# Performance work log

Hardware: AMD Instinct MI355X
Metric: run time of the kernel (lower is better)

The kernel has to match this reference:

```python
import jax, jax.numpy as jnp
import numpy as np

DIM = 1024
HEADS = 16
HEAD_DIM = DIM // HEADS          # 64
ROT_DIM = max(16, HEAD_DIM // 2) # 32 (already even)
B, S = 1, 2048


def _linear_params(key, scale=0.02):
    w = jax.random.normal(key, (DIM, DIM), dtype=jnp.float32) * scale
    b = jnp.zeros((DIM,), dtype=jnp.float32)
    return w, b


def setup_inputs() -> dict:
    key = jax.random.key(0)
    ks = jax.random.split(key, 16)
    real = jax.random.normal(ks[0], (B, S, DIM), dtype=jnp.float32)
    imag = jax.random.normal(ks[1], (B, S, DIM), dtype=jnp.float32)
    Wq_r, bq_r = _linear_params(ks[2])
    Wk_r, bk_r = _linear_params(ks[3])
    Wv_r, bv_r = _linear_params(ks[4])
    Wq_i, bq_i = _linear_params(ks[5])
    Wk_i, bk_i = _linear_params(ks[6])
    Wv_i, bv_i = _linear_params(ks[7])
    Wo_r, bo_r = _linear_params(ks[8])
    Wo_i, bo_i = _linear_params(ks[9])
    phase_shifts = jax.random.normal(ks[10], (HEADS, HEAD_DIM), dtype=jnp.float32) * 0.02
    # entanglement init: 0.8*I + 0.1 on super/sub diagonal + 0.1 corners
    ent = np.eye(HEADS, dtype=np.float32) * 0.8
    ent += np.diag(np.ones(HEADS - 1, dtype=np.float32) * 0.1, k=1)
    ent += np.diag(np.ones(HEADS - 1, dtype=np.float32) * 0.1, k=-1)
    ent[0, -1] = 0.1
    ent[-1, 0] = 0.1
    entanglement_matrix = jnp.asarray(ent)
    exponent = np.arange(0, ROT_DIM, 2, dtype=np.float64) / ROT_DIM
    rotary_freqs = jnp.asarray((10000.0 ** (-exponent)).astype(np.float32))
    return {
        'real': real, 'imag': imag,
        'Wq_r': Wq_r, 'bq_r': bq_r, 'Wk_r': Wk_r, 'bk_r': bk_r,
        'Wv_r': Wv_r, 'bv_r': bv_r, 'Wq_i': Wq_i, 'bq_i': bq_i,
        'Wk_i': Wk_i, 'bk_i': bk_i, 'Wv_i': Wv_i, 'bv_i': bv_i,
        'Wo_r': Wo_r, 'bo_r': bo_r, 'Wo_i': Wo_i, 'bo_i': bo_i,
        'phase_shifts': phase_shifts,
        'entanglement_matrix': entanglement_matrix,
        'rotary_freqs': rotary_freqs,
        'interference_strength': jnp.float32(0.0),
        'attention_temperature': jnp.float32(0.0),
        'circle_epsilon': jnp.float32(-2.0),
    }


def _proj(x, W, b):
    # nn.Linear: x @ W^T + b, then split heads -> [B,H,S,Dh]
    y = x @ W.T + b
    return y.reshape(B, S, HEADS, HEAD_DIM).transpose(0, 2, 1, 3)


def _rope(x, cos, sin):
    # x: [B,H,S,Dh]; interleaved pairs rotated over first ROT_DIM dims
    xr, xp = x[..., :ROT_DIM], x[..., ROT_DIM:]
    x1, x2 = xr[..., 0::2], xr[..., 1::2]          # [B,H,S,ROT_DIM//2]
    o1 = x1 * cos - x2 * sin
    o2 = x1 * sin + x2 * cos
    out = jnp.stack([o1, o2], axis=-1).reshape(x.shape[:-1] + (ROT_DIM,))
    return jnp.concatenate([out, xp], axis=-1)


def reference(real, imag, Wq_r, bq_r, Wk_r, bk_r, Wv_r, bv_r,
              Wq_i, bq_i, Wk_i, bk_i, Wv_i, bv_i,
              Wo_r, bo_r, Wo_i, bo_i,
              phase_shifts, entanglement_matrix, rotary_freqs,
              interference_strength, attention_temperature, circle_epsilon):
    q_r = _proj(real, Wq_r, bq_r)
    k_r = _proj(real, Wk_r, bk_r)
    v_r = _proj(real, Wv_r, bv_r)
    q_i = _proj(imag, Wq_i, bq_i)
    k_i = _proj(imag, Wk_i, bk_i)
    v_i = _proj(imag, Wv_i, bv_i)

    # rotary embeddings
    pos = jnp.arange(S, dtype=jnp.float32)
    angles = jnp.outer(pos, rotary_freqs)              # [S, ROT_DIM//2]
    cos = jnp.cos(angles)[None, None]                  # [1,1,S,ROT_DIM//2]
    sin = jnp.sin(angles)[None, None]
    q_r = _rope(q_r, cos, sin); k_r = _rope(k_r, cos, sin)
    q_i = _rope(q_i, cos, sin); k_i = _rope(k_i, cos, sin)

    # entanglement mixing across heads
    q_r = jnp.einsum('bhsd,hx->bxsd', q_r, entanglement_matrix)
    q_i = jnp.einsum('bhsd,hx->bxsd', q_i, entanglement_matrix)
    k_r = jnp.einsum('bhsd,hx->bxsd', k_r, entanglement_matrix)
    k_i = jnp.einsum('bhsd,hx->bxsd', k_i, entanglement_matrix)

    # per-head learned phase shift
    pc = jnp.cos(phase_shifts)[None, :, None, :]       # [1,H,1,Dh]
    ps = jnp.sin(phase_shifts)[None, :, None, :]
    q_r, q_i = q_r * pc - q_i * ps, q_r * ps + q_i * pc
    k_r, k_i = k_r * pc - k_i * ps, k_r * ps + k_i * pc

    # complex attention scores (Karatsuba, as in HAKMEMComplexOperations)
    scale = 1.0 / np.sqrt(HEAD_DIM)
    k1 = jnp.einsum('bhsd,bhtd->bhst', q_r, k_r)
    k2 = jnp.einsum('bhsd,bhtd->bhst', q_i, k_i)
    k3 = jnp.einsum('bhsd,bhtd->bhst', q_r + q_i, k_r + k_i)
    attn_r = (k1 - k2) * scale
    attn_i = (k3 - k1 - k2) * scale

    eps = jax.nn.sigmoid(circle_epsilon) * 0.03
    ar = attn_r + eps * attn_i
    ai = attn_i - eps * attn_r
    attn_mag = jnp.sqrt(ar * ar + ai * ai + 1e-6)

    causal = jnp.triu(jnp.ones((S, S), dtype=bool), k=1)[None, None]
    attn_mag = jnp.where(causal, -jnp.inf, attn_mag)

    temp = jnp.clip(jnp.exp(attention_temperature), 0.1, None)
    strength = jax.nn.sigmoid(interference_strength)
    attn = jax.nn.softmax(attn_mag * strength / temp, axis=-1)
    attn = jnp.nan_to_num(attn)

    # complex_matmul(attn, 0, v_r, v_i) -> (attn@v_r, attn@v_i)
    out_r = jnp.einsum('bhst,bhtd->bhsd', attn, v_r)
    out_i = jnp.einsum('bhst,bhtd->bhsd', attn, v_i)
    out_r = out_r.transpose(0, 2, 1, 3).reshape(B, S, DIM)
    out_i = out_i.transpose(0, 2, 1, 3).reshape(B, S, DIM)
    out_r = out_r @ Wo_r.T + bo_r
    out_i = out_i @ Wo_i.T + bo_i
    return out_r, out_i
```

## Files before the change

### kernel.cpp

```cpp
#include <hip/hip_runtime.h>
#include <cstddef>
#include <cstdint>
#include <math.h>

#define S_LEN 2048
#define DIM 1024
#define NH 16
#define HD 64

typedef __attribute__((ext_vector_type(8))) short bf16x8;
typedef __attribute__((ext_vector_type(8))) unsigned short u16x8;
typedef __attribute__((ext_vector_type(4))) float f32x4;

__device__ inline unsigned short f2bf(float x) {
  union { float f; unsigned u; } v; v.f = x;
  unsigned r = v.u + 0x7FFFu + ((v.u >> 16) & 1u);
  return (unsigned short)(r >> 16);
}
__device__ inline float bf2f(unsigned short x) {
  union { unsigned u; float f; } v; v.u = ((unsigned)x) << 16; return v.f;
}

#define GLOAD_LDS16(g, l)                                              \
  __builtin_amdgcn_global_load_lds(                                    \
      (const __attribute__((address_space(1))) void*)(g),              \
      (__attribute__((address_space(3))) void*)(l), 16, 0, 0)

struct ConvBatch {
  const float* src[10];
  unsigned short* dst[10];
  int n[10];
};

__global__ __launch_bounds__(256) void conv_kernel(ConvBatch cb)
{
  const int y = blockIdx.y;
  const int i = (blockIdx.x * 256 + threadIdx.x) * 8;
  if (i >= cb.n[y]) return;
  const float* s = cb.src[y];
  float4 a = *(const float4*)(s + i);
  float4 b = *(const float4*)(s + i + 4);
  u16x8 o;
  o[0] = f2bf(a.x); o[1] = f2bf(a.y); o[2] = f2bf(a.z); o[3] = f2bf(a.w);
  o[4] = f2bf(b.x); o[5] = f2bf(b.y); o[6] = f2bf(b.z); o[7] = f2bf(b.w);
  *(u16x8*)(cb.dst[y] + i) = o;
}

struct BGemm {
  const unsigned short* A[6];
  const unsigned short* W[6];
  const float* bias[6];
  void* C[6];
  int mode[6];
};

__global__ __launch_bounds__(256) void gemm_mfma_kernel(BGemm gb)
{
  constexpr int K = DIM;
  const int z = blockIdx.z;
  const unsigned short* __restrict__ A = gb.A[z];
  const unsigned short* __restrict__ W = gb.W[z];
  const float* __restrict__ bias = gb.bias[z];
  const int mode = gb.mode[z];

  __shared__ __align__(16) unsigned short As[128 * 32];
  __shared__ __align__(16) unsigned short Ws[128 * 32];

  const int t    = threadIdx.x;
  const int lane = t & 63;
  const int w    = t >> 6;
  const int wm   = w >> 1, wn = w & 1;
  const int quad = lane >> 4, lcol = lane & 15;
  const int m0   = blockIdx.y * 128;
  const int n0   = blockIdx.x * 128;

  const int srow = t >> 2;
  const int sk8  = (t & 3) * 8;

  f32x4 acc[4][4];
#pragma unroll
  for (int i = 0; i < 4; i++)
#pragma unroll
    for (int j = 0; j < 4; j++)
#pragma unroll
      for (int r = 0; r < 4; r++) acc[i][j][r] = 0.f;

  for (int k0 = 0; k0 < K; k0 += 32) {
    __syncthreads();
#pragma unroll
    for (int p = 0; p < 2; p++) {
      const unsigned short* ga = A + (size_t)(m0 + p * 64 + srow) * K + k0 + sk8;
      GLOAD_LDS16(ga, As + (size_t)(p * 256 + w * 64) * 8);
      const unsigned short* gw = W + (size_t)(n0 + p * 64 + srow) * K + k0 + sk8;
      GLOAD_LDS16(gw, Ws + (size_t)(p * 256 + w * 64) * 8);
    }
    __syncthreads();

    bf16x8 af[4], bfr[4];
#pragma unroll
    for (int mi = 0; mi < 4; mi++)
      af[mi] = *(const bf16x8*)&As[(wm * 64 + mi * 16 + lcol) * 32 + quad * 8];
#pragma unroll
    for (int ni = 0; ni < 4; ni++)
      bfr[ni] = *(const bf16x8*)&Ws[(wn * 64 + ni * 16 + lcol) * 32 + quad * 8];
#pragma unroll
    for (int mi = 0; mi < 4; mi++)
#pragma unroll
      for (int ni = 0; ni < 4; ni++)
        acc[mi][ni] = __builtin_amdgcn_mfma_f32_16x16x32_bf16(af[mi], bfr[ni], acc[mi][ni], 0, 0, 0);
  }

#pragma unroll
  for (int mi = 0; mi < 4; mi++) {
#pragma unroll
    for (int ni = 0; ni < 4; ni++) {
#pragma unroll
      for (int r = 0; r < 4; r++) {
        const int grow = m0 + wm * 64 + mi * 16 + quad * 4 + r;
        const int gcol = n0 + wn * 64 + ni * 16 + lcol;
        const float v = acc[mi][ni][r] + bias[gcol];
        if (mode == 0) {
          ((float*)gb.C[z])[(size_t)grow * DIM + gcol] = v;
        } else if (mode == 1) {
          const int hh = gcol >> 6, d = gcol & 63;
          ((unsigned short*)gb.C[z])[((size_t)hh * S_LEN + grow) * HD + d] = f2bf(v);
        } else {
          const int hh = gcol >> 6, d = gcol & 63;
          ((unsigned short*)gb.C[z])[((size_t)hh * HD + d) * S_LEN + grow] = f2bf(v);
        }
      }
    }
  }
}

__global__ __launch_bounds__(256) void rope_kernel(
    unsigned short* q_r, unsigned short* k_r,
    unsigned short* q_i, unsigned short* k_i,
    const float* __restrict__ freqs)
{
  const int gid = blockIdx.x * 256 + threadIdx.x;
  const int j  = gid & 15;
  const int s  = (gid >> 4) & (S_LEN - 1);
  const int h  = (gid >> 15) & (NH - 1);
  const int tz = gid >> 19;
  unsigned short* buf = (tz == 0) ? q_r : (tz == 1) ? k_r : (tz == 2) ? q_i : k_i;

  const float ang = (float)s * freqs[j];
  float sn, cs;
  sincosf(ang, &sn, &cs);

  const size_t base = ((size_t)h * S_LEN + s) * HD + 2 * j;
  ushort2 xv = *(const ushort2*)(buf + base);
  const float x1 = bf2f(xv.x), x2 = bf2f(xv.y);
  ushort2 ov;
  ov.x = f2bf(x1 * cs - x2 * sn);
  ov.y = f2bf(x1 * sn + x2 * cs);
  *(ushort2*)(buf + base) = ov;
}

__global__ __launch_bounds__(256) void entangle_kernel(
    const unsigned short* __restrict__ qr_in, const unsigned short* __restrict__ qi_in,
    unsigned short* __restrict__ qr_out, unsigned short* __restrict__ qi_out,
    const unsigned short* __restrict__ kr_in, const unsigned short* __restrict__ ki_in,
    unsigned short* __restrict__ kr_out, unsigned short* __restrict__ ki_out,
    const float* __restrict__ E, const float* __restrict__ phase)
{
  const int z = blockIdx.z;
  const unsigned short* inR = z ? kr_in : qr_in;
  const unsigned short* inI = z ? ki_in : qi_in;
  unsigned short* outR = z ? kr_out : qr_out;
  unsigned short* outI = z ? ki_out : qi_out;

  __shared__ float Es[NH * NH];
  const int t = threadIdx.x;
  Es[t] = E[t];
  __syncthreads();

  const int idx = blockIdx.x * 256 + t;
  const int s = idx >> 6;
  const int d = idx & 63;

  float vr[NH], vi[NH];
#pragma unroll
  for (int h = 0; h < NH; h++) {
    const size_t off = ((size_t)h * S_LEN + s) * HD + d;
    vr[h] = bf2f(inR[off]);
    vi[h] = bf2f(inI[off]);
  }

#pragma unroll
  for (int x = 0; x < NH; x++) {
    float er = 0.f, ei = 0.f;
#pragma unroll
    for (int h = 0; h < NH; h++) {
      const float e = Es[h * NH + x];
      er += vr[h] * e;
      ei += vi[h] * e;
    }
    const float ph = phase[x * HD + d];
    float ps, pc;
    sincosf(ph, &ps, &pc);
    const size_t off = ((size_t)x * S_LEN + s) * HD + d;
    outR[off] = f2bf(er * pc - ei * ps);
    outI[off] = f2bf(er * ps + ei * pc);
  }
}

#define LDK 72

__global__ __launch_bounds__(256) void flash_mfma_kernel(
    const unsigned short* __restrict__ Qr, const unsigned short* __restrict__ Qi,
    const unsigned short* __restrict__ Kr, const unsigned short* __restrict__ Ki,
    const unsigned short* __restrict__ VtR, const unsigned short* __restrict__ VtI,
    unsigned short* __restrict__ Or, unsigned short* __restrict__ Oi,
    const float* __restrict__ p_is, const float* __restrict__ p_at,
    const float* __restrict__ p_ce)
{
  __shared__ __align__(16) unsigned short Krs[64 * LDK];
  __shared__ __align__(16) unsigned short Kis[64 * LDK];
  __shared__ __align__(16) unsigned short VTr[64 * LDK];
  __shared__ __align__(16) unsigned short VTi[64 * LDK];
  __shared__ __align__(16) unsigned short Ps [64 * LDK];

  const int t    = threadIdx.x;
  const int lane = t & 63;
  const int w    = t >> 6;
  const int quad = lane >> 4;
  const int lcol = lane & 15;

  const int L    = blockIdx.x;
  const int c    = L & 255;
  const int h    = c & 15;
  const int base = c >> 4;
  const int itile = (L >> 8) ? (31 - base) : base;
  const int i0   = itile * 64;
  const int ntiles = itile + 1;

  const float strength = 1.f / (1.f + expf(-p_is[0]));
  const float temp     = fmaxf(expf(p_at[0]), 0.1f);
  const float cfac     = strength / temp;
  const float eps      = 0.03f / (1.f + expf(-p_ce[0]));
  const float c2       = 0.015625f * (1.f + eps * eps);

  const int srow = t >> 3;
  const int sd0  = (t & 7) * 8;

  bf16x8 qrf[2], qif[2];
  {
    const int qrow = i0 + w * 16 + lcol;
    const size_t base_q = ((size_t)h * S_LEN + qrow) * HD;
#pragma unroll
    for (int ks = 0; ks < 2; ks++) {
      qrf[ks] = *(const bf16x8*)(Qr + base_q + ks * 32 + quad * 8);
      qif[ks] = *(const bf16x8*)(Qi + base_q + ks * 32 + quad * 8);
    }
  }

  float lsum[4] = {0.f, 0.f, 0.f, 0.f};
  f32x4 aOr[4], aOi[4];
#pragma unroll
  for (int cc = 0; cc < 4; cc++)
#pragma unroll
    for (int r = 0; r < 4; r++) { aOr[cc][r] = 0.f; aOi[cc][r] = 0.f; }

  bf16x8 pk[2], pki[2], pv[2], pvi[2];

  {
    const size_t kb = ((size_t)h * S_LEN) * HD;
#pragma unroll
    for (int it = 0; it < 2; it++) {
      const int row = srow + it * 32;
      pk [it] = *(const bf16x8*)(Kr  + kb + (size_t)row * HD + sd0);
      pki[it] = *(const bf16x8*)(Ki  + kb + (size_t)row * HD + sd0);
      pv [it] = *(const bf16x8*)(VtR + ((size_t)h * HD + row) * S_LEN + sd0);
      pvi[it] = *(const bf16x8*)(VtI + ((size_t)h * HD + row) * S_LEN + sd0);
    }
  }

  for (int jt = 0; jt < ntiles; jt++) {
    __syncthreads();
#pragma unroll
    for (int it = 0; it < 2; it++) {
      const int row = srow + it * 32;
      *(bf16x8*)&Krs[row * LDK + sd0] = pk [it];
      *(bf16x8*)&Kis[row * LDK + sd0] = pki[it];
      *(bf16x8*)&VTr[row * LDK + sd0] = pv [it];
      *(bf16x8*)&VTi[row * LDK + sd0] = pvi[it];
    }
    __syncthreads();

    if (jt + 1 < ntiles) {
      const int j0n = (jt + 1) * 64;
      const size_t kb = ((size_t)h * S_LEN + j0n) * HD;
#pragma unroll
      for (int it = 0; it < 2; it++) {
        const int row = srow + it * 32;
        pk [it] = *(const bf16x8*)(Kr  + kb + (size_t)row * HD + sd0);
        pki[it] = *(const bf16x8*)(Ki  + kb + (size_t)row * HD + sd0);
        pv [it] = *(const bf16x8*)(VtR + ((size_t)h * HD + row) * S_LEN + j0n + sd0);
        pvi[it] = *(const bf16x8*)(VtI + ((size_t)h * HD + row) * S_LEN + j0n + sd0);
      }
    }

    f32x4 k1[4], k2[4], kx[4];
#pragma unroll
    for (int cc = 0; cc < 4; cc++)
#pragma unroll
      for (int r = 0; r < 4; r++) { k1[cc][r] = 0.f; k2[cc][r] = 0.f; kx[cc][r] = 0.f; }
#pragma unroll
    for (int ks = 0; ks < 2; ks++) {
#pragma unroll
      for (int cc = 0; cc < 4; cc++) {
        const int off = (cc * 16 + lcol) * LDK + ks * 32 + quad * 8;
        bf16x8 krf = *(const bf16x8*)&Krs[off];
        bf16x8 kif = *(const bf16x8*)&Kis[off];
        k1[cc] = __builtin_amdgcn_mfma_f32_16x16x32_bf16(qrf[ks], krf, k1[cc], 0, 0, 0);
        k2[cc] = __builtin_amdgcn_mfma_f32_16x16x32_bf16(qif[ks], kif, k2[cc], 0, 0, 0);
        kx[cc] = __builtin_amdgcn_mfma_f32_16x16x32_bf16(qrf[ks], kif, kx[cc], 0, 0, 0);
        kx[cc] = __builtin_amdgcn_mfma_f32_16x16x32_bf16(qif[ks], krf, kx[cc], 0, 0, 0);
      }
    }

    const bool diag = (jt == ntiles - 1);
    const int j0 = jt * 64;
#pragma unroll
    for (int r = 0; r < 4; r++) {
      const int prow = (w * 16 + quad * 4 + r) * LDK;
      float rs = 0.f;
#pragma unroll
      for (int cc = 0; cc < 4; cc++) {
        const float a = k1[cc][r] - k2[cc][r];
        const float b = kx[cc][r];
        const float u = fmaf(b, b, a * a);
        const float mag = sqrtf(fmaf(u, c2, 1e-6f));
        float p = __expf(mag * cfac);
        if (diag) {
          const int gi = i0 + w * 16 + quad * 4 + r;
          const int gj = j0 + cc * 16 + lcol;
          if (gj > gi) p = 0.f;
        }
        Ps[prow + cc * 16 + lcol] = f2bf(p);
        rs += p;
      }
      lsum[r] += rs;
    }

#pragma unroll
    for (int ks = 0; ks < 2; ks++) {
      bf16x8 pf = *(const bf16x8*)&Ps[(w * 16 + lcol) * LDK + ks * 32 + quad * 8];
#pragma unroll
      for (int cc = 0; cc < 4; cc++) {
        const int off = (cc * 16 + lcol) * LDK + ks * 32 + quad * 8;
        bf16x8 vrf = *(const bf16x8*)&VTr[off];
        bf16x8 vif = *(const bf16x8*)&VTi[off];
        aOr[cc] = __builtin_amdgcn_mfma_f32_16x16x32_bf16(pf, vrf, aOr[cc], 0, 0, 0);
        aOi[cc] = __builtin_amdgcn_mfma_f32_16x16x32_bf16(pf, vif, aOi[cc], 0, 0, 0);
      }
    }
  }

  float inv[4];
#pragma unroll
  for (int r = 0; r < 4; r++) {
    float rs = lsum[r];
#pragma unroll
    for (int off = 1; off < 16; off <<= 1)
      rs += __shfl_xor(rs, off, 16);
    inv[r] = 1.f / rs;
  }

#pragma unroll
  for (int cc = 0; cc < 4; cc++) {
#pragma unroll
    for (int r = 0; r < 4; r++) {
      const int row = i0 + w * 16 + quad * 4 + r;
      const int col = h * HD + cc * 16 + lcol;
      Or[(size_t)row * DIM + col] = f2bf(aOr[cc][r] * inv[r]);
      Oi[(size_t)row * DIM + col] = f2bf(aOi[cc][r] * inv[r]);
    }
  }
}

extern "C" void kernel_launch(void* const* d_in, const int* in_sizes, int n_in,
                              void* d_out, int out_size, void* d_ws, size_t ws_size,
                              hipStream_t stream)
{
  const float* real = (const float*)d_in[0];
  const float* imag = (const float*)d_in[1];
  const float* Wq_r = (const float*)d_in[2];
  const float* bq_r = (const float*)d_in[3];
  const float* Wk_r = (const float*)d_in[4];
  const float* bk_r = (const float*)d_in[5];
  const float* Wv_r = (const float*)d_in[6];
  const float* bv_r = (const float*)d_in[7];
  const float* Wq_i = (const float*)d_in[8];
  const float* bq_i = (const float*)d_in[9];
  const float* Wk_i = (const float*)d_in[10];
  const float* bk_i = (const float*)d_in[11];
  const float* Wv_i = (const float*)d_in[12];
  const float* bv_i = (const float*)d_in[13];
  const float* Wo_r = (const float*)d_in[14];
  const float* bo_r = (const float*)d_in[15];
  const float* Wo_i = (const float*)d_in[16];
  const float* bo_i = (const float*)d_in[17];
  const float* phase = (const float*)d_in[18];
  const float* ent   = (const float*)d_in[19];
  const float* freqs = (const float*)d_in[20];
  const float* p_is  = (const float*)d_in[21];
  const float* p_at  = (const float*)d_in[22];
  const float* p_ce  = (const float*)d_in[23];

  unsigned short* ws = (unsigned short*)d_ws;
  const size_t SL = (size_t)S_LEN * DIM;
  const size_t WL = (size_t)DIM * DIM;

  unsigned short* realb = ws;
  unsigned short* imagb = realb + SL;
  unsigned short* Wb    = imagb + SL;
  unsigned short* q_r   = Wb + 8 * WL;
  unsigned short* k_r   = q_r + SL;
  unsigned short* v_r   = k_r + SL;
  unsigned short* q_i   = v_r + SL;
  unsigned short* k_i   = q_i + SL;
  unsigned short* v_i   = k_i + SL;
  unsigned short* Qr    = v_i + SL;
  unsigned short* Qi    = Qr + SL;
  unsigned short* Kr    = Qi + SL;
  unsigned short* Ki    = Kr + SL;
  unsigned short* O_r   = q_r;
  unsigned short* O_i   = q_i;

  float* out_r = (float*)d_out;
  float* out_i = out_r + SL;

  ConvBatch cb;
  cb.src[0] = real; cb.dst[0] = realb; cb.n[0] = (int)SL;
  cb.src[1] = imag; cb.dst[1] = imagb; cb.n[1] = (int)SL;
  const float* wsrc[8] = {Wq_r, Wk_r, Wv_r, Wq_i, Wk_i, Wv_i, Wo_r, Wo_i};
  for (int i = 0; i < 8; i++) {
    cb.src[2 + i] = wsrc[i];
    cb.dst[2 + i] = Wb + (size_t)i * WL;
    cb.n[2 + i] = (int)WL;
  }
  conv_kernel<<<dim3(1024, 10), dim3(256), 0, stream>>>(cb);

  BGemm g1;
  g1.A[0] = realb; g1.A[1] = realb; g1.A[2] = realb;
  g1.A[3] = imagb; g1.A[4] = imagb; g1.A[5] = imagb;
  for (int i = 0; i < 6; i++) g1.W[i] = Wb + (size_t)i * WL;
  g1.bias[0] = bq_r; g1.bias[1] = bk_r; g1.bias[2] = bv_r;
  g1.bias[3] = bq_i; g1.bias[4] = bk_i; g1.bias[5] = bv_i;
  g1.C[0] = q_r; g1.C[1] = k_r; g1.C[2] = v_r;
  g1.C[3] = q_i; g1.C[4] = k_i; g1.C[5] = v_i;
  g1.mode[0] = 1; g1.mode[1] = 1; g1.mode[2] = 2;
  g1.mode[3] = 1; g1.mode[4] = 1; g1.mode[5] = 2;
  gemm_mfma_kernel<<<dim3(8, 16, 6), dim3(256), 0, stream>>>(g1);

  rope_kernel<<<dim3(8192), dim3(256), 0, stream>>>(q_r, k_r, q_i, k_i, freqs);

  entangle_kernel<<<dim3(512, 1, 2), dim3(256), 0, stream>>>(
      q_r, q_i, Qr, Qi, k_r, k_i, Kr, Ki, ent, phase);

  flash_mfma_kernel<<<dim3(512), dim3(256), 0, stream>>>(
      Qr, Qi, Kr, Ki, v_r, v_i, O_r, O_i, p_is, p_at, p_ce);

  BGemm g2 = {};
  g2.A[0] = O_r; g2.A[1] = O_i;
  g2.W[0] = Wb + 6 * WL; g2.W[1] = Wb + 7 * WL;
  g2.bias[0] = bo_r; g2.bias[1] = bo_i;
  g2.C[0] = out_r; g2.C[1] = out_i;
  g2.mode[0] = 0; g2.mode[1] = 0;
  gemm_mfma_kernel<<<dim3(8, 16, 2), dim3(256), 0, stream>>>(g2);
}
```

Before: 304.3 us.

## Fold entanglement into Q/K weights, table RoPE/phase, split flash attention KV range

Moves the head-entanglement mix off the activations and into the Q and K projection weights and biases during conversion, which removes the separate entangle kernel and its extra buffers. RoPE and the phase rotation are merged into one vectorized kernel that reads precomputed sin/cos tables. Flash attention now splits each query tile's key range into two halves across blocks to balance the causal workload, and a combine kernel sums the fp32 partial outputs and row sums. This relies on RoPE commuting with the head mix, since both act per position and per dimension. It adds fp32 partial-output traffic and an extra launch.

After: 308.3 us. Within noise of the previous version (+1.3%).

```diff
diff --git a/kernel.cpp b/kernel.cpp
--- a/kernel.cpp
+++ b/kernel.cpp
@@ -30,20 +30,87 @@
   const float* src[10];
   unsigned short* dst[10];
   int n[10];
+  int fold[10];
 };
 
-__global__ __launch_bounds__(256) void conv_kernel(ConvBatch cb)
-{
+__global__ __launch_bounds__(256) void conv_kernel(ConvBatch cb,
+                                                   const float* __restrict__ E)
+{
+  __shared__ float Es[NH * NH];
+  const int t = threadIdx.x;
+  Es[t] = E[t];
+  __syncthreads();
+
   const int y = blockIdx.y;
-  const int i = (blockIdx.x * 256 + threadIdx.x) * 8;
-  if (i >= cb.n[y]) return;
+  const int flat = (blockIdx.x * 256 + t) * 8;
+  if (flat >= cb.n[y]) return;
   const float* s = cb.src[y];
-  float4 a = *(const float4*)(s + i);
-  float4 b = *(const float4*)(s + i + 4);
-  u16x8 o;
-  o[0] = f2bf(a.x); o[1] = f2bf(a.y); o[2] = f2bf(a.z); o[3] = f2bf(a.w);
-  o[4] = f2bf(b.x); o[5] = f2bf(b.y); o[6] = f2bf(b.z); o[7] = f2bf(b.w);
-  *(u16x8*)(cb.dst[y] + i) = o;
+
+  if (!cb.fold[y]) {
+    float4 a = *(const float4*)(s + flat);
+    float4 b = *(const float4*)(s + flat + 4);
+    u16x8 o;
+    o[0] = f2bf(a.x); o[1] = f2bf(a.y); o[2] = f2bf(a.z); o[3] = f2bf(a.w);
+    o[4] = f2bf(b.x); o[5] = f2bf(b.y); o[6] = f2bf(b.z); o[7] = f2bf(b.w);
+    *(u16x8*)(cb.dst[y] + flat) = o;
+  } else {
+    const int row = flat >> 10;
+    const int k0  = flat & 1023;
+    const int x = row >> 6, d = row & 63;
+    float acc[8] = {};
+#pragma unroll
+    for (int h = 0; h < NH; h++) {
+      const float e = Es[h * NH + x];
+      const float* p = s + ((size_t)((h << 6) + d) << 10) + k0;
+      float4 a = *(const float4*)p;
+      float4 b = *(const float4*)(p + 4);
+      acc[0] += e * a.x; acc[1] += e * a.y; acc[2] += e * a.z; acc[3] += e * a.w;
+      acc[4] += e * b.x; acc[5] += e * b.y; acc[6] += e * b.z; acc[7] += e * b.w;
+    }
+    u16x8 o;
+#pragma unroll
+    for (int j = 0; j < 8; j++) o[j] = f2bf(acc[j]);
+    *(u16x8*)(cb.dst[y] + flat) = o;
+  }
+}
+
+__global__ __launch_bounds__(256) void bias_fold_kernel(
+    const float* __restrict__ b0, const float* __restrict__ b1,
+    const float* __restrict__ b2, const float* __restrict__ b3,
+    const float* __restrict__ E, float* __restrict__ out)
+{
+  __shared__ float Es[NH * NH];
+  const int t = threadIdx.x;
+  Es[t] = E[t];
+  __syncthreads();
+  const float* srcs[4] = {b0, b1, b2, b3};
+  for (int idx = t; idx < 4096; idx += 256) {
+    const int tz = idx >> 10, nn = idx & 1023;
+    const int x = nn >> 6, d = nn & 63;
+    const float* b = srcs[tz];
+    float acc = 0.f;
+#pragma unroll
+    for (int h = 0; h < NH; h++) acc += Es[h * NH + x] * b[h * 64 + d];
+    out[idx] = acc;
+  }
+}
+
+__global__ __launch_bounds__(256) void prep_tabs_kernel(
+    const float* __restrict__ freqs, const float* __restrict__ phase,
+    float2* __restrict__ ropeTab, float2* __restrict__ phaseTab)
+{
+  const int idx = blockIdx.x * 256 + threadIdx.x;
+  if (idx < 32768) {
+    const int s = idx >> 4, j = idx & 15;
+    float sn, cs;
+    sincosf((float)s * freqs[j], &sn, &cs);
+    ropeTab[idx] = make_float2(cs, sn);
+  } else if (idx < 32768 + 1024) {
+    const int k = idx - 32768;
+    float sn, cs;
+    sincosf(phase[k], &sn, &cs);
+    phaseTab[k] = make_float2(cs, sn);
+  }
 }
 
 struct BGemm {
@@ -133,77 +200,54 @@
   }
 }
 
-__global__ __launch_bounds__(256) void rope_kernel(
-    unsigned short* q_r, unsigned short* k_r,
-    unsigned short* q_i, unsigned short* k_i,
-    const float* __restrict__ freqs)
-{
-  const int gid = blockIdx.x * 256 + threadIdx.x;
-  const int j  = gid & 15;
-  const int s  = (gid >> 4) & (S_LEN - 1);
-  const int h  = (gid >> 15) & (NH - 1);
-  const int tz = gid >> 19;
-  unsigned short* buf = (tz == 0) ? q_r : (tz == 1) ? k_r : (tz == 2) ? q_i : k_i;
-
-  const float ang = (float)s * freqs[j];
-  float sn, cs;
-  sincosf(ang, &sn, &cs);
-
-  const size_t base = ((size_t)h * S_LEN + s) * HD + 2 * j;
-  ushort2 xv = *(const ushort2*)(buf + base);
-  const float x1 = bf2f(xv.x), x2 = bf2f(xv.y);
-  ushort2 ov;
-  ov.x = f2bf(x1 * cs - x2 * sn);
-  ov.y = f2bf(x1 * sn + x2 * cs);
-  *(ushort2*)(buf + base) = ov;
-}
-
-__global__ __launch_bounds__(256) void entangle_kernel(
-    const unsigned short* __restrict__ qr_in, const unsigned short* __restrict__ qi_in,
-    unsigned short* __restrict__ qr_out, unsigned short* __restrict__ qi_out,
-    const unsigned short* __restrict__ kr_in, const unsigned short* __restrict__ ki_in,
-    unsigned short* __restrict__ kr_out, unsigned short* __restrict__ ki_out,
-    const float* __restrict__ E, const float* __restrict__ phase)
-{
-  const int z = blockIdx.z;
-  const unsigned short* inR = z ? kr_in : qr_in;
-  const unsigned short* inI = z ? ki_in : qi_in;
-  unsigned short* outR = z ? kr_out : qr_out;
-  unsigned short* outI = z ? ki_out : qi_out;
-
-  __shared__ float Es[NH * NH];
-  const int t = threadIdx.x;
-  Es[t] = E[t];
-  __syncthreads();
-
-  const int idx = blockIdx.x * 256 + t;
-  const int s = idx >> 6;
-  const int d = idx & 63;
-
-  float vr[NH], vi[NH];
-#pragma unroll
-  for (int h = 0; h < NH; h++) {
-    const size_t off = ((size_t)h * S_LEN + s) * HD + d;
-    vr[h] = bf2f(inR[off]);
-    vi[h] = bf2f(inI[off]);
-  }
-
-#pragma unroll
-  for (int x = 0; x < NH; x++) {
-    float er = 0.f, ei = 0.f;
-#pragma unroll
-    for (int h = 0; h < NH; h++) {
-      const float e = Es[h * NH + x];
-      er += vr[h] * e;
-      ei += vi[h] * e;
-    }
-    const float ph = phase[x * HD + d];
-    float ps, pc;
-    sincosf(ph, &ps, &pc);
-    const size_t off = ((size_t)x * S_LEN + s) * HD + d;
-    outR[off] = f2bf(er * pc - ei * ps);
-    outI[off] = f2bf(er * ps + ei * pc);
-  }
+__global__ __launch_bounds__(256) void ropephase_kernel(
+    unsigned short* q_r, unsigned short* q_i,
+    unsigned short* k_r, unsigned short* k_i,
+    const float2* __restrict__ ropeTab, const float2* __restrict__ phaseTab)
+{
+  const int z = blockIdx.y;
+  unsigned short* R = z ? k_r : q_r;
+  unsigned short* I = z ? k_i : q_i;
+
+  const int flat = blockIdx.x * 256 + threadIdx.x;
+  const int x   = flat >> 14;
+  const int rem = flat & 16383;
+  const int s   = rem >> 3;
+  const int d0  = (rem & 7) * 8;
+
+  const size_t base = ((size_t)x * S_LEN + s) * HD + d0;
+  bf16x8 r8 = *(const bf16x8*)(R + base);
+  bf16x8 i8 = *(const bf16x8*)(I + base);
+  float a[8], b[8];
+#pragma unroll
+  for (int e = 0; e < 8; e++) {
+    a[e] = bf2f((unsigned short)r8[e]);
+    b[e] = bf2f((unsigned short)i8[e]);
+  }
+
+  if (d0 < 32) {
+#pragma unroll
+    for (int jj = 0; jj < 8; jj += 2) {
+      const int j = (d0 + jj) >> 1;
+      const float2 cs = ropeTab[s * 16 + j];
+      const float a1 = a[jj], a2 = a[jj + 1];
+      const float b1 = b[jj], b2 = b[jj + 1];
+      a[jj]     = a1 * cs.x - a2 * cs.y;
+      a[jj + 1] = a1 * cs.y + a2 * cs.x;
+      b[jj]     = b1 * cs.x - b2 * cs.y;
+      b[jj + 1] = b1 * cs.y + b2 * cs.x;
+    }
+  }
+
+  u16x8 orr, oii;
+#pragma unroll
+  for (int e = 0; e < 8; e++) {
+    const float2 pp = phaseTab[x * HD + d0 + e];
+    orr[e] = f2bf(a[e] * pp.x - b[e] * pp.y);
+    oii[e] = f2bf(a[e] * pp.y + b[e] * pp.x);
+  }
+  *(u16x8*)(R + base) = orr;
+  *(u16x8*)(I + base) = oii;
 }
 
 #define LDK 72
@@ -212,7 +256,7 @@
     const unsigned short* __restrict__ Qr, const unsigned short* __restrict__ Qi,
     const unsigned short* __restrict__ Kr, const unsigned short* __restrict__ Ki,
     const unsigned short* __restrict__ VtR, const unsigned short* __restrict__ VtI,
-    unsigned short* __restrict__ Or, unsigned short* __restrict__ Oi,
+    float* __restrict__ OpR, float* __restrict__ OpI, float* __restrict__ Lp,
     const float* __restrict__ p_is, const float* __restrict__ p_at,
     const float* __restrict__ p_ce)
 {
@@ -228,13 +272,16 @@
   const int quad = lane >> 4;
   const int lcol = lane & 15;
 
-  const int L    = blockIdx.x;
-  const int c    = L & 255;
-  const int h    = c & 15;
-  const int base = c >> 4;
-  const int itile = (L >> 8) ? (31 - base) : base;
-  const int i0   = itile * 64;
-  const int ntiles = itile + 1;
+  const int bx    = blockIdx.x;
+  const int p     = bx >> 1;
+  const int half  = bx & 1;
+  const int itile = 31 - (p >> 4);
+  const int h     = p & 15;
+  const int i0    = itile * 64;
+  const int n     = itile + 1;
+  const int jmid  = (n + 1) >> 1;
+  const int jbeg  = half ? jmid : 0;
+  const int jend  = half ? n : jmid;
 
   const float strength = 1.f / (1.f + expf(-p_is[0]));
   const float temp     = fmaxf(expf(p_at[0]), 0.1f);
@@ -265,19 +312,20 @@
 
   bf16x8 pk[2], pki[2], pv[2], pvi[2];
 
-  {
-    const size_t kb = ((size_t)h * S_LEN) * HD;
+  if (jbeg < jend) {
+    const int j0 = jbeg * 64;
+    const size_t kb = ((size_t)h * S_LEN + j0) * HD;
 #pragma unroll
     for (int it = 0; it < 2; it++) {
       const int row = srow + it * 32;
       pk [it] = *(const bf16x8*)(Kr  + kb + (size_t)row * HD + sd0);
       pki[it] = *(const bf16x8*)(Ki  + kb + (size_t)row * HD + sd0);
-      pv [it] = *(const bf16x8*)(VtR + ((size_t)h * HD + row) * S_LEN + sd0);
-      pvi[it] = *(const bf16x8*)(VtI + ((size_t)h * HD + row) * S_LEN + sd0);
-    }
-  }
-
-  for (int jt = 0; jt < ntiles; jt++) {
+      pv [it] = *(const bf16x8*)(VtR + ((size_t)h * HD + row) * S_LEN + j0 + sd0);
+      pvi[it] = *(const bf16x8*)(VtI + ((size_t)h * HD + row) * S_LEN + j0 + sd0);
+    }
+  }
+
+  for (int jt = jbeg; jt < jend; jt++) {
     __syncthreads();
 #pragma unroll
     for (int it = 0; it < 2; it++) {
@@ -289,7 +337,7 @@
     }
     __syncthreads();
 
-    if (jt + 1 < ntiles) {
+    if (jt + 1 < jend) {
       const int j0n = (jt + 1) * 64;
       const size_t kb = ((size_t)h * S_LEN + j0n) * HD;
 #pragma unroll
@@ -321,7 +369,7 @@
       }
     }
 
-    const bool diag = (jt == ntiles - 1);
+    const bool diag = (jt == itile);
     const int j0 = jt * 64;
 #pragma unroll
     for (int r = 0; r < 4; r++) {
@@ -333,14 +381,14 @@
         const float b = kx[cc][r];
         const float u = fmaf(b, b, a * a);
         const float mag = sqrtf(fmaf(u, c2, 1e-6f));
-        float p = __expf(mag * cfac);
+        float pp = __expf(mag * cfac);
         if (diag) {
           const int gi = i0 + w * 16 + quad * 4 + r;
           const int gj = j0 + cc * 16 + lcol;
-          if (gj > gi) p = 0.f;
+          if (gj > gi) pp = 0.f;
         }
-        Ps[prow + cc * 16 + lcol] = f2bf(p);
-        rs += p;
+        Ps[prow + cc * 16 + lcol] = f2bf(pp);
+        rs += pp;
       }
       lsum[r] += rs;
     }
@@ -359,26 +407,56 @@
     }
   }
 
-  float inv[4];
+  const size_t SLsz = (size_t)S_LEN * DIM;
 #pragma unroll
   for (int r = 0; r < 4; r++) {
     float rs = lsum[r];
 #pragma unroll
     for (int off = 1; off < 16; off <<= 1)
       rs += __shfl_xor(rs, off, 16);
-    inv[r] = 1.f / rs;
-  }
-
+    const int row = i0 + w * 16 + quad * 4 + r;
+    if (lcol == 0)
+      Lp[((size_t)half * NH + h) * S_LEN + row] = rs;
+  }
 #pragma unroll
   for (int cc = 0; cc < 4; cc++) {
 #pragma unroll
     for (int r = 0; r < 4; r++) {
       const int row = i0 + w * 16 + quad * 4 + r;
       const int col = h * HD + cc * 16 + lcol;
-      Or[(size_t)row * DIM + col] = f2bf(aOr[cc][r] * inv[r]);
-      Oi[(size_t)row * DIM + col] = f2bf(aOi[cc][r] * inv[r]);
-    }
-  }
+      OpR[half * SLsz + (size_t)row * DIM + col] = aOr[cc][r];
+      OpI[half * SLsz + (size_t)row * DIM + col] = aOi[cc][r];
+    }
+  }
+}
+
+__global__ __launch_bounds__(256) void combine_kernel(
+    const float* __restrict__ OpR, const float* __restrict__ OpI,
+    const float* __restrict__ Lp,
+    unsigned short* __restrict__ Or, unsigned short* __restrict__ Oi)
+{
+  const size_t SLsz = (size_t)S_LEN * DIM;
+  const int idx = blockIdx.x * 256 + threadIdx.x;
+  const size_t e0 = (size_t)idx * 4;
+  const int s = (int)(e0 >> 10);
+  const int col = (int)(e0 & 1023);
+  const int h = col >> 6;
+
+  const float L = Lp[(size_t)h * S_LEN + s] + Lp[((size_t)NH + h) * S_LEN + s];
+  const float inv = 1.f / L;
+
+  float4 r0 = *(const float4*)(OpR + e0);
+  float4 r1 = *(const float4*)(OpR + SLsz + e0);
+  float4 i0 = *(const float4*)(OpI + e0);
+  float4 i1 = *(const float4*)(OpI + SLsz + e0);
+
+  ushort4 orv, oiv;
+  orv.x = f2bf((r0.x + r1.x) * inv); orv.y = f2bf((r0.y + r1.y) * inv);
+  orv.z = f2bf((r0.z + r1.z) * inv); orv.w = f2bf((r0.w + r1.w) * inv);
+  oiv.x = f2bf((i0.x + i1.x) * inv); oiv.y = f2bf((i0.y + i1.y) * inv);
+  oiv.z = f2bf((i0.z + i1.z) * inv); oiv.w = f2bf((i0.w + i1.w) * inv);
+  *(ushort4*)(Or + e0) = orv;
+  *(ushort4*)(Oi + e0) = oiv;
 }
 
 extern "C" void kernel_launch(void* const* d_in, const int* in_sizes, int n_in,
@@ -423,46 +501,58 @@
   unsigned short* q_i   = v_r + SL;
   unsigned short* k_i   = q_i + SL;
   unsigned short* v_i   = k_i + SL;
-  unsigned short* Qr    = v_i + SL;
-  unsigned short* Qi    = Qr + SL;
-  unsigned short* Kr    = Qi + SL;
-  unsigned short* Ki    = Kr + SL;
-  unsigned short* O_r   = q_r;
-  unsigned short* O_i   = q_i;
+
+  float* fbase   = (float*)(v_i + SL);
+  float* biasf   = fbase;
+  float* ropeTab = biasf + 4096;
+  float* phaseTb = ropeTab + 65536;
+  float* OpR     = phaseTb + 2048;
+  float* OpI     = OpR + 2 * SL;
+  float* Lp      = OpI + 2 * SL;
+
+  unsigned short* O_r = q_r;
+  unsigned short* O_i = q_i;
 
   float* out_r = (float*)d_out;
   float* out_i = out_r + SL;
 
   ConvBatch cb;
-  cb.src[0] = real; cb.dst[0] = realb; cb.n[0] = (int)SL;
-  cb.src[1] = imag; cb.dst[1] = imagb; cb.n[1] = (int)SL;
+  cb.src[0] = real; cb.dst[0] = realb; cb.n[0] = (int)SL; cb.fold[0] = 0;
+  cb.src[1] = imag; cb.dst[1] = imagb; cb.n[1] = (int)SL; cb.fold[1] = 0;
   const float* wsrc[8] = {Wq_r, Wk_r, Wv_r, Wq_i, Wk_i, Wv_i, Wo_r, Wo_i};
+  const int wfold[8]   = {1,    1,    0,    1,    1,    0,    0,    0};
   for (int i = 0; i < 8; i++) {
     cb.src[2 + i] = wsrc[i];
     cb.dst[2 + i] = Wb + (size_t)i * WL;
     cb.n[2 + i] = (int)WL;
-  }
-  conv_kernel<<<dim3(1024, 10), dim3(256), 0, stream>>>(cb);
+    cb.fold[2 + i] = wfold[i];
+  }
+  conv_kernel<<<dim3(1024, 10), dim3(256), 0, stream>>>(cb, ent);
+
+  bias_fold_kernel<<<dim3(1), dim3(256), 0, stream>>>(bq_r, bk_r, bq_i, bk_i, ent, biasf);
+
+  prep_tabs_kernel<<<dim3(132), dim3(256), 0, stream>>>(
+      freqs, phase, (float2*)ropeTab, (float2*)phaseTb);
 
   BGemm g1;
   g1.A[0] = realb; g1.A[1] = realb; g1.A[2] = realb;
   g1.A[3] = imagb; g1.A[4] = imagb; g1.A[5] = imagb;
   for (int i = 0; i < 6; i++) g1.W[i] = Wb + (size_t)i * WL;
-  g1.bias[0] = bq_r; g1.bias[1] = bk_r; g1.bias[2] = bv_r;
-  g1.bias[3] = bq_i; g1.bias[4] = bk_i; g1.bias[5] = bv_i;
+  g1.bias[0] = biasf;        g1.bias[1] = biasf + 1024; g1.bias[2] = bv_r;
+  g1.bias[3] = biasf + 2048; g1.bias[4] = biasf + 3072; g1.bias[5] = bv_i;
   g1.C[0] = q_r; g1.C[1] = k_r; g1.C[2] = v_r;
   g1.C[3] = q_i; g1.C[4] = k_i; g1.C[5] = v_i;
   g1.mode[0] = 1; g1.mode[1] = 1; g1.mode[2] = 2;
   g1.mode[3] = 1; g1.mode[4] = 1; g1.mode[5] = 2;
   gemm_mfma_kernel<<<dim3(8, 16, 6), dim3(256), 0, stream>>>(g1);
 
-  rope_kernel<<<dim3(8192), dim3(256), 0, stream>>>(q_r, k_r, q_i, k_i, freqs);
-
-  entangle_kernel<<<dim3(512, 1, 2), dim3(256), 0, stream>>>(
-      q_r, q_i, Qr, Qi, k_r, k_i, Kr, Ki, ent, phase);
-
-  flash_mfma_kernel<<<dim3(512), dim3(256), 0, stream>>>(
-      Qr, Qi, Kr, Ki, v_r, v_i, O_r, O_i, p_is, p_at, p_ce);
+  ropephase_kernel<<<dim3(1024, 2), dim3(256), 0, stream>>>(
+      q_r, q_i, k_r, k_i, (const float2*)ropeTab, (const float2*)phaseTb);
+
+  flash_mfma_kernel<<<dim3(1024), dim3(256), 0, stream>>>(
+      q_r, q_i, k_r, k_i, v_r, v_i, OpR, OpI, Lp, p_is, p_at, p_ce);
+
+  combine_kernel<<<dim3(2048), dim3(256), 0, stream>>>(OpR, OpI, Lp, O_r, O_i);
 
   BGemm g2 = {};
   g2.A[0] = O_r; g2.A[1] = O_i;
```
